# Kernel tuning notes

Measured on AMD Instinct MI355X. Metric: run time of the kernel, lower is better.

## Reference

```python
import jax, jax.numpy as jnp
import numpy as np

GRID = 20          # visual_cortex_mask is an all-True GRID^3 volume -> S = 8000 active voxels
NUM_NEIGHBORS = 32
FEATURE_DIM = 512
NUM_HEADS = 8
BATCH = 4


def _knn_indices():
    # Coordinates of all active voxels in flat (active-order) indexing.
    zz, yy, xx = np.meshgrid(np.arange(GRID), np.arange(GRID), np.arange(GRID), indexing='ij')
    coords = np.stack([zz.ravel(), yy.ravel(), xx.ravel()], axis=1).astype(np.float32)  # [S,3]
    sq = (coords ** 2).sum(-1)
    d2 = sq[:, None] + sq[None, :] - 2.0 * (coords @ coords.T)  # squared distances [S,S]
    np.fill_diagonal(d2, np.inf)  # exclude self, mirrors nearest[:, 1:]
    nbr = np.argpartition(d2, NUM_NEIGHBORS - 1, axis=1)[:, :NUM_NEIGHBORS]
    return nbr.astype(np.int32)  # [S, K] positions in active-voxel order


def setup_inputs() -> dict:
    key = jax.random.key(0)
    k1, k2, k3, k4 = jax.random.split(key, 4)
    S = GRID ** 3
    x = jax.random.normal(k1, (BATCH, S, FEATURE_DIM), dtype=jnp.float32)
    scale = 0.02
    Wq = jax.random.normal(k2, (FEATURE_DIM, FEATURE_DIM), dtype=jnp.float32) * scale
    Wk = jax.random.normal(k3, (FEATURE_DIM, FEATURE_DIM), dtype=jnp.float32) * scale
    Wv = jax.random.normal(k4, (FEATURE_DIM, FEATURE_DIM), dtype=jnp.float32) * scale
    nbr = jnp.asarray(_knn_indices())
    return {"x": x, "Wq": Wq, "Wk": Wk, "Wv": Wv, "nbr": nbr}


def reference(x, Wq, Wk, Wv, nbr):
    B, S, F = x.shape
    H = NUM_HEADS
    Hd = F // H

    def proj(W):
        # nn.Linear(bias=False): x @ W.T, then split heads -> [B, H, S, Hd]
        return (x @ W.T).reshape(B, S, H, Hd).transpose(0, 2, 1, 3)

    q = proj(Wq)
    k = proj(Wk)
    v = proj(Wv)

    # Gather each query's fixed-size neighbor K/V set: [B, H, S, K, Hd].
    # Exactly equivalent to the flex_attention KNN mask (neighbor set == allowed kv set).
    kn = k[:, :, nbr, :]
    vn = v[:, :, nbr, :]

    scores = jnp.einsum('bhsd,bhskd->bhsk', q, kn) * (Hd ** -0.5)
    w = jax.nn.softmax(scores, axis=-1)
    out = jnp.einsum('bhsk,bhskd->bhsd', w, vn)  # [B, H, S, Hd]
    return out.transpose(0, 2, 1, 3).reshape(B, S, F)
```

## Files before the change

### kernel.cpp

```cpp
#include <hip/hip_runtime.h>
#include <cstddef>
#include <cstdint>

#define GRID_S 8000
#define FDIM 512
#define NHEAD 8
#define HD 64
#define KNN 32
#define NB 4
#define M_TOT (NB * GRID_S)

typedef __attribute__((ext_vector_type(8))) __bf16 bf16x8;
typedef __attribute__((ext_vector_type(4))) float f32x4;
typedef __attribute__((ext_vector_type(2))) float f32x2;
typedef __attribute__((ext_vector_type(2))) short short2v;

#if __has_builtin(__builtin_elementwise_fma)
#define FMA2(a,b,c) __builtin_elementwise_fma((a),(b),(c))
#else
#define FMA2(a,b,c) ((a)*(b)+(c))
#endif

#if __has_builtin(__builtin_amdgcn_fdot2_f32_bf16)
#define HAS_DOT2 1
#else
#define HAS_DOT2 0
#endif

__device__ inline ushort f2bf(float f) {
    uint32_t u = __builtin_bit_cast(uint32_t, f);
    uint32_t r = (u + 0x7fffu + ((u >> 16) & 1u)) >> 16;
    return (ushort)r;
}
__device__ inline f32x2 unpk(uint32_t u) {
    f32x2 r;
    r.x = __builtin_bit_cast(float, u << 16);
    r.y = __builtin_bit_cast(float, u & 0xffff0000u);
    return r;
}

#define NX4 (M_TOT * FDIM / 4)
#define NW4 (FDIM * FDIM / 4)

__global__ __launch_bounds__(256) void cvt_all(const float* __restrict__ x,
                                               const float* __restrict__ Wq,
                                               const float* __restrict__ Wk,
                                               const float* __restrict__ Wv,
                                               ushort* __restrict__ xb,
                                               ushort* __restrict__ wb) {
    int i = blockIdx.x * 256 + threadIdx.x;
    if (i < NX4) {
        float4 f = ((const float4*)x)[i];
        ushort4 o = { f2bf(f.x), f2bf(f.y), f2bf(f.z), f2bf(f.w) };
        ((ushort4*)xb)[i] = o;
        return;
    }
    i -= NX4;
    const int which = i >> 16;
    const int off = i & (NW4 - 1);
    const float* w = (which == 0) ? Wq : (which == 1) ? Wk : Wv;
    float4 f = ((const float4*)w)[off];
    ushort4 o = { f2bf(f.x), f2bf(f.y), f2bf(f.z), f2bf(f.w) };
    ((ushort4*)wb)[which * NW4 + off] = o;
}

#define TBM 128
#define TBN 128
#define TBK 64

__device__ inline void gload_lds16(const ushort* g, ushort* l) {
    __builtin_amdgcn_global_load_lds((const __attribute__((address_space(1))) uint32_t*)g,
                                     (__attribute__((address_space(3))) uint32_t*)l,
                                     16, 0, 0);
}

__global__ __launch_bounds__(256) void gemm_qkv(const ushort* __restrict__ A,
                                                const ushort* __restrict__ B,
                                                ushort* __restrict__ qo,
                                                ushort* __restrict__ kvo) {
    __shared__ ushort As[TBM * TBK];
    __shared__ ushort Bs[TBN * TBK];
    const int tid = threadIdx.x;
    const int wv = tid >> 6;
    const int lane = tid & 63;
    const int bm = blockIdx.x * TBM;
    const int bn = blockIdx.y * TBN;
    const int wr = (wv >> 1) * 64;
    const int wc = (wv & 1) * 64;
    f32x4 acc[4][4] = {};

    const int srow = wv * 32 + (lane >> 3);
    const int scol = (lane & 7) * 8;
    const int fr = lane & 15;
    const int fk = (lane >> 4) * 8;

    for (int k0 = 0; k0 < FDIM; k0 += TBK) {
        const ushort* ga = A + (size_t)(bm + srow) * FDIM + k0 + scol;
        const ushort* gb = B + (size_t)(bn + srow) * FDIM + k0 + scol;
        #pragma unroll
        for (int r = 0; r < 4; ++r) {
            gload_lds16(ga + (size_t)(8 * r) * FDIM, &As[(wv * 32 + 8 * r) * TBK]);
            gload_lds16(gb + (size_t)(8 * r) * FDIM, &Bs[(wv * 32 + 8 * r) * TBK]);
        }
        __syncthreads();

        #pragma unroll
        for (int kk = 0; kk < 2; ++kk) {
            bf16x8 af[4], bfr[4];
            #pragma unroll
            for (int i = 0; i < 4; ++i) {
                af[i]  = *(const bf16x8*)&As[(wr + i * 16 + fr) * TBK + kk * 32 + fk];
                bfr[i] = *(const bf16x8*)&Bs[(wc + i * 16 + fr) * TBK + kk * 32 + fk];
            }
            #pragma unroll
            for (int i = 0; i < 4; ++i)
                #pragma unroll
                for (int j = 0; j < 4; ++j)
                    acc[i][j] = __builtin_amdgcn_mfma_f32_16x16x32_bf16(af[i], bfr[j], acc[i][j], 0, 0, 0);
        }
        __syncthreads();
    }

    const int cr = (lane >> 4) * 4;
    const int cc = lane & 15;
    const int seg = blockIdx.y >> 2;
    const int cn = (blockIdx.y & 3) * TBN;
    if (seg == 0) {
        #pragma unroll
        for (int i = 0; i < 4; ++i)
            #pragma unroll
            for (int j = 0; j < 4; ++j) {
                ushort* cp = qo + (size_t)(bm + wr + i * 16 + cr) * FDIM + cn + wc + j * 16 + cc;
                #pragma unroll
                for (int r = 0; r < 4; ++r)
                    cp[(size_t)r * FDIM] = f2bf(acc[i][j][r] * 0.125f);
            }
    } else {
        ushort* base = kvo + ((seg == 2) ? FDIM : 0);
        #pragma unroll
        for (int i = 0; i < 4; ++i)
            #pragma unroll
            for (int j = 0; j < 4; ++j) {
                ushort* cp = base + (size_t)(bm + wr + i * 16 + cr) * (2 * FDIM) + cn + wc + j * 16 + cc;
                #pragma unroll
                for (int r = 0; r < 4; ++r)
                    cp[(size_t)r * (2 * FDIM)] = f2bf(acc[i][j][r]);
            }
    }
}

__global__ __launch_bounds__(256) void knn_attn10(const ushort* __restrict__ q,
                                                  const ushort* __restrict__ kv,
                                                  const int* __restrict__ nbr,
                                                  float* __restrict__ out) {
    const int bid = blockIdx.x;
    const int base = ((bid & 7) * (M_TOT / 32) + (bid >> 3)) * 4;
    const int lane = threadIdx.x & 63;
    const int wv = threadIdx.x >> 6;
    const int bs = base + wv;
    const int b = bs / GRID_S;
    const int s = bs - b * GRID_S;
    const int* __restrict__ nrow = nbr + s * KNN;

    const uint4 qw = *(const uint4*)(q + (size_t)bs * FDIM + 8 * lane);
#if HAS_DOT2
    const short2v qs0 = __builtin_bit_cast(short2v, qw.x);
    const short2v qs1 = __builtin_bit_cast(short2v, qw.y);
    const short2v qs2 = __builtin_bit_cast(short2v, qw.z);
    const short2v qs3 = __builtin_bit_cast(short2v, qw.w);
#else
    const f32x2 q2[4] = { unpk(qw.x), unpk(qw.y), unpk(qw.z), unpk(qw.w) };
#endif

    const ushort* kvb = kv + (size_t)b * GRID_S * (2 * FDIM) + 8 * lane;

#if HAS_DOT2
#define SCORE1(kw, p)                                                                     \
    p = __builtin_amdgcn_fdot2_f32_bf16(__builtin_bit_cast(short2v, kw.x), qs0, 0.f, false); \
    p = __builtin_amdgcn_fdot2_f32_bf16(__builtin_bit_cast(short2v, kw.y), qs1, p, false);   \
    p = __builtin_amdgcn_fdot2_f32_bf16(__builtin_bit_cast(short2v, kw.z), qs2, p, false);   \
    p = __builtin_amdgcn_fdot2_f32_bf16(__builtin_bit_cast(short2v, kw.w), qs3, p, false);   \
    p += __shfl_xor(p, 1); p += __shfl_xor(p, 2); p += __shfl_xor(p, 4);
#else
#define SCORE1(kw, p)                                                                     \
    {                                                                                     \
        f32x2 a2 = q2[0] * unpk(kw.x);                                                    \
        a2 = FMA2(q2[1], unpk(kw.y), a2);                                                 \
        a2 = FMA2(q2[2], unpk(kw.z), a2);                                                 \
        a2 = FMA2(q2[3], unpk(kw.w), a2);                                                 \
        p = a2.x + a2.y;                                                                  \
    }                                                                                     \
    p += __shfl_xor(p, 1); p += __shfl_xor(p, 2); p += __shfl_xor(p, 4);
#endif

    uint4 kbuf[3], vbuf[3];
    #pragma unroll
    for (int t = 0; t < 3; ++t) {
        const ushort* rp = kvb + ((size_t)(uint32_t)nrow[t] << 10);
        kbuf[t] = *(const uint4*)rp;
        vbuf[t] = *(const uint4*)(rp + FDIM);
    }

    float m, sum;
    f32x2 acc[4];
    {
        float p;
        SCORE1(kbuf[0], p);
        m = p;
        sum = 1.f;
        acc[0] = unpk(vbuf[0].x);
        acc[1] = unpk(vbuf[0].y);
        acc[2] = unpk(vbuf[0].z);
        acc[3] = unpk(vbuf[0].w);
    }
    #pragma unroll
    for (int j = 1; j < KNN; ++j) {
        if (j + 2 < KNN) {
            const ushort* rp = kvb + ((size_t)(uint32_t)nrow[j + 2] << 10);
            kbuf[(j + 2) % 3] = *(const uint4*)rp;
            vbuf[(j + 2) % 3] = *(const uint4*)(rp + FDIM);
        }
        const uint4 kw = kbuf[j % 3];
        const uint4 vw = vbuf[j % 3];
        float p;
        SCORE1(kw, p);
        if (__any(p - m > 8.f)) {
            const float nm = fmaxf(m, p);
            const float c = __expf(m - nm);
            const f32x2 c2 = {c, c};
            sum *= c;
            acc[0] *= c2; acc[1] *= c2; acc[2] *= c2; acc[3] *= c2;
            m = nm;
        }
        const float w = __expf(p - m);
        sum += w;
        const f32x2 w2 = {w, w};
        acc[0] = FMA2(w2, unpk(vw.x), acc[0]);
        acc[1] = FMA2(w2, unpk(vw.y), acc[1]);
        acc[2] = FMA2(w2, unpk(vw.z), acc[2]);
        acc[3] = FMA2(w2, unpk(vw.w), acc[3]);
    }

    const float inv = 1.0f / sum;
    const f32x2 inv2 = {inv, inv};
    #pragma unroll
    for (int r = 0; r < 4; ++r) acc[r] *= inv2;

    float* op = out + (size_t)bs * FDIM + 8 * lane;
    float4 o0 = {acc[0].x, acc[0].y, acc[1].x, acc[1].y};
    float4 o1 = {acc[2].x, acc[2].y, acc[3].x, acc[3].y};
    *(float4*)op = o0;
    *(float4*)(op + 4) = o1;
#undef SCORE1
}

extern "C" void kernel_launch(void* const* d_in, const int* in_sizes, int n_in,
                              void* d_out, int out_size, void* d_ws, size_t ws_size,
                              hipStream_t stream) {
    const float* x  = (const float*)d_in[0];
    const float* Wq = (const float*)d_in[1];
    const float* Wk = (const float*)d_in[2];
    const float* Wv = (const float*)d_in[3];
    const int*   nbr = (const int*)d_in[4];
    float* out = (float*)d_out;

    const size_t m_elems = (size_t)M_TOT * FDIM;
    const size_t w_elems = (size_t)FDIM * FDIM;

    ushort* xb  = (ushort*)d_ws;
    ushort* wb  = xb + m_elems;
    ushort* kvb = wb + 3 * w_elems;
    ushort* qbf = kvb + 2 * m_elems;

    cvt_all<<<(NX4 + 3 * NW4) / 256, 256, 0, stream>>>(x, Wq, Wk, Wv, xb, wb);

    dim3 grid(M_TOT / TBM, 3 * FDIM / TBN);
    gemm_qkv<<<grid, 256, 0, stream>>>(xb, wb, qbf, kvb);

    knn_attn10<<<M_TOT / 4, 256, 0, stream>>>(qbf, kvb, nbr, out);
}
```

Before: 198.9 us.

## Fuse fp32-to-bf16 conversion of x into QKV GEMM tile loads

The separate pass that converted x to bf16 in a workspace is removed. The GEMM now reads fp32 x directly, converts it in registers and stores it to LDS, so only the weights are still pre-converted. The grid is also transposed so the 12 column blocks sharing one row tile of x launch together, which helps L2 reuse of the fp32 rows. The catch is that each x tile is now read as fp32 (twice the bytes) by all 12 column blocks, and loads become synchronous register loads instead of direct-to-LDS loads.

```diff
diff --git a/kernel.cpp b/kernel.cpp
--- a/kernel.cpp
+++ b/kernel.cpp
@@ -39,23 +39,13 @@
     return r;
 }
 
-#define NX4 (M_TOT * FDIM / 4)
 #define NW4 (FDIM * FDIM / 4)
 
-__global__ __launch_bounds__(256) void cvt_all(const float* __restrict__ x,
-                                               const float* __restrict__ Wq,
-                                               const float* __restrict__ Wk,
-                                               const float* __restrict__ Wv,
-                                               ushort* __restrict__ xb,
-                                               ushort* __restrict__ wb) {
-    int i = blockIdx.x * 256 + threadIdx.x;
-    if (i < NX4) {
-        float4 f = ((const float4*)x)[i];
-        ushort4 o = { f2bf(f.x), f2bf(f.y), f2bf(f.z), f2bf(f.w) };
-        ((ushort4*)xb)[i] = o;
-        return;
-    }
-    i -= NX4;
+__global__ __launch_bounds__(256) void cvt_w(const float* __restrict__ Wq,
+                                             const float* __restrict__ Wk,
+                                             const float* __restrict__ Wv,
+                                             ushort* __restrict__ wb) {
+    const int i = blockIdx.x * 256 + threadIdx.x;
     const int which = i >> 16;
     const int off = i & (NW4 - 1);
     const float* w = (which == 0) ? Wq : (which == 1) ? Wk : Wv;
@@ -74,8 +64,8 @@
                                      16, 0, 0);
 }
 
-__global__ __launch_bounds__(256) void gemm_qkv(const ushort* __restrict__ A,
-                                                const ushort* __restrict__ B,
+__global__ __launch_bounds__(256) void gemm_qkv(const float* __restrict__ X,
+                                                const ushort* __restrict__ Bw,
                                                 ushort* __restrict__ qo,
                                                 ushort* __restrict__ kvo) {
     __shared__ ushort As[TBM * TBK];
@@ -83,8 +73,8 @@
     const int tid = threadIdx.x;
     const int wv = tid >> 6;
     const int lane = tid & 63;
-    const int bm = blockIdx.x * TBM;
-    const int bn = blockIdx.y * TBN;
+    const int bm = blockIdx.y * TBM;
+    const int bn = blockIdx.x * TBN;
     const int wr = (wv >> 1) * 64;
     const int wc = (wv & 1) * 64;
     f32x4 acc[4][4] = {};
@@ -95,12 +85,22 @@
     const int fk = (lane >> 4) * 8;
 
     for (int k0 = 0; k0 < FDIM; k0 += TBK) {
-        const ushort* ga = A + (size_t)(bm + srow) * FDIM + k0 + scol;
-        const ushort* gb = B + (size_t)(bn + srow) * FDIM + k0 + scol;
+        const ushort* gb = Bw + (size_t)(bn + srow) * FDIM + k0 + scol;
+        #pragma unroll
+        for (int r = 0; r < 4; ++r)
+            gload_lds16(gb + (size_t)(8 * r) * FDIM, &Bs[(wv * 32 + 8 * r) * TBK]);
+
+        const float* ga = X + (size_t)(bm + srow) * FDIM + k0 + scol;
         #pragma unroll
         for (int r = 0; r < 4; ++r) {
-            gload_lds16(ga + (size_t)(8 * r) * FDIM, &As[(wv * 32 + 8 * r) * TBK]);
-            gload_lds16(gb + (size_t)(8 * r) * FDIM, &Bs[(wv * 32 + 8 * r) * TBK]);
+            const float4 f0 = *(const float4*)(ga + (size_t)(8 * r) * FDIM);
+            const float4 f1 = *(const float4*)(ga + (size_t)(8 * r) * FDIM + 4);
+            bf16x8 pk;
+            pk[0] = (__bf16)f0.x; pk[1] = (__bf16)f0.y;
+            pk[2] = (__bf16)f0.z; pk[3] = (__bf16)f0.w;
+            pk[4] = (__bf16)f1.x; pk[5] = (__bf16)f1.y;
+            pk[6] = (__bf16)f1.z; pk[7] = (__bf16)f1.w;
+            *(bf16x8*)&As[(srow + 8 * r) * TBK + scol] = pk;
         }
         __syncthreads();
 
@@ -123,8 +123,8 @@
 
     const int cr = (lane >> 4) * 4;
     const int cc = lane & 15;
-    const int seg = blockIdx.y >> 2;
-    const int cn = (blockIdx.y & 3) * TBN;
+    const int seg = blockIdx.x >> 2;
+    const int cn = (blockIdx.x & 3) * TBN;
     if (seg == 0) {
         #pragma unroll
         for (int i = 0; i < 4; ++i)
@@ -267,15 +267,14 @@
     const size_t m_elems = (size_t)M_TOT * FDIM;
     const size_t w_elems = (size_t)FDIM * FDIM;
 
-    ushort* xb  = (ushort*)d_ws;
-    ushort* wb  = xb + m_elems;
+    ushort* wb  = (ushort*)d_ws;
     ushort* kvb = wb + 3 * w_elems;
     ushort* qbf = kvb + 2 * m_elems;
 
-    cvt_all<<<(NX4 + 3 * NW4) / 256, 256, 0, stream>>>(x, Wq, Wk, Wv, xb, wb);
-
-    dim3 grid(M_TOT / TBM, 3 * FDIM / TBN);
-    gemm_qkv<<<grid, 256, 0, stream>>>(xb, wb, qbf, kvb);
+    cvt_w<<<3 * NW4 / 256, 256, 0, stream>>>(Wq, Wk, Wv, wb);
+
+    dim3 grid(3 * FDIM / TBN, M_TOT / TBM);
+    gemm_qkv<<<grid, 256, 0, stream>>>(x, wb, qbf, kvb);
 
     knn_attn10<<<M_TOT / 4, 256, 0, stream>>>(qbf, kvb, nbr, out);
 }
```

Result: slower. 207.5 us (+4.3%).
